# Performance work log

Measured on AMD Instinct MI355X. Metric: run time of the kernel, lower is better.

The kernel has to match this reference:

```python
import jax, jax.numpy as jnp
import numpy as np

B, N, D, H, C = 32, 512, 256, 256, 2
EPS_NEIGH = 0.3
VSN = 1e-12
SMOOTH_R, DEGREE_R, SPARSITY_R = 0.2, 0.0, 0.1


def setup_inputs() -> dict:
    key = jax.random.key(0)
    ks = jax.random.split(key, 12)
    s = 0.02
    return {
        "context": jax.random.normal(ks[0], (B, N, D), jnp.float32),
        "attention_mask": jnp.ones((B, N, 1), jnp.int32),
        "W_gcn": jax.random.normal(ks[1], (D, H), jnp.float32) * s,
        "b_gcn": jnp.zeros((H,), jnp.float32),
        "W_att1": jax.random.normal(ks[2], (H, H), jnp.float32) * s,
        "b_att1": jnp.zeros((H,), jnp.float32),
        "ln_g": jnp.ones((H,), jnp.float32),
        "ln_b": jnp.zeros((H,), jnp.float32),
        "W_att2": jax.random.normal(ks[3], (H, 1), jnp.float32) * s,
        "b_att2": jnp.zeros((1,), jnp.float32),
        "W_out": jax.random.normal(ks[4], (H, C), jnp.float32) * s,
        "b_out": jnp.zeros((C,), jnp.float32),
    }


def reference(context, attention_mask, W_gcn, b_gcn, W_att1, b_att1,
              ln_g, ln_b, W_att2, b_att2, W_out, b_out):
    # --- GraphLearner (cosine metric + epsilon neighbourhood) ---
    cn = context / jnp.maximum(
        jnp.linalg.norm(context, axis=-1, keepdims=True), VSN)
    att = jnp.einsum('bnd,bmd->bnm', cn, cn)              # [B,N,N]
    mask = jax.lax.stop_gradient((att > EPS_NEIGH).astype(att.dtype))
    adj = att * mask                                      # markoff_value = 0

    # --- GCN diffusion (row-normalized adjacency) ---
    row = adj.sum(-1, keepdims=True)                      # [B,N,1]
    adj_norm = adj / (row + VSN)
    h = jax.nn.relu(
        jnp.einsum('bnm,bmd->bnd', adj_norm, context) @ W_gcn + b_gcn)

    # --- AttentionNetPooling: Linear -> LayerNorm -> GELU -> Linear(1) ---
    a = h @ W_att1 + b_att1
    mu = a.mean(-1, keepdims=True)
    var = a.var(-1, keepdims=True)
    a = (a - mu) / jnp.sqrt(var + 1e-5) * ln_g + ln_b
    w = jax.nn.gelu(a, approximate=False) @ W_att2 + b_att2   # [B,N,1]
    w = jnp.where(attention_mask == 0, -jnp.inf, w)
    w = jax.nn.softmax(w, axis=1)
    pooled = jnp.sum(w * h, axis=1)                       # [B,H]
    logits = pooled @ W_out + b_out                       # [B,C]

    # --- add_batch_graph_loss (L = diag(rowsum) - adj, topk = N) ---
    Lx = row * context - jnp.einsum('bnm,bmd->bnd', adj, context)
    smooth = SMOOTH_R * jnp.mean(
        jnp.sum(context * Lx, axis=(-1, -2)) / (N * N))
    deg = -DEGREE_R * jnp.mean(
        jnp.sum(jnp.log(row[..., 0] + VSN), axis=-1) / N)
    sparsity = SPARSITY_R * jnp.sum(adj ** 2) / (N * N) / B
    graph_loss = smooth + deg + sparsity
    return logits, graph_loss
```

## Files before the change

### kernel.cpp

```cpp
#include <hip/hip_runtime.h>
#include <math.h>

#define NS 512
#define ND 256
#define LIST_CAP 32768u

typedef short short8 __attribute__((ext_vector_type(8)));
typedef float f32x16 __attribute__((ext_vector_type(16)));

__device__ __forceinline__ unsigned short bf16_rne(float x) {
  unsigned u = __float_as_uint(x);
  unsigned r = u + 0x7fffu + ((u >> 16) & 1u);
  return (unsigned short)(r >> 16);
}
__device__ __forceinline__ float bf16_tof(unsigned short h) {
  return __uint_as_float(((unsigned)h) << 16);
}
__device__ __forceinline__ void bsplit(float x, unsigned short& h, unsigned short& l) {
  h = bf16_rne(x);
  l = bf16_rne(x - bf16_tof(h));
}
__device__ __forceinline__ float wave_sum(float v) {
  v += __shfl_xor(v, 1);  v += __shfl_xor(v, 2);  v += __shfl_xor(v, 4);
  v += __shfl_xor(v, 8);  v += __shfl_xor(v, 16); v += __shfl_xor(v, 32);
  return v;
}

__device__ __forceinline__ void gload_lds16(const void* g, void* l) {
  __builtin_amdgcn_global_load_lds(
      (const __attribute__((address_space(1))) unsigned int*)g,
      (__attribute__((address_space(3))) unsigned int*)l, 16, 0, 0);
}

__device__ __forceinline__ void stage4(const unsigned short* __restrict__ hiA,
                                       const unsigned short* __restrict__ loA, int grA,
                                       const unsigned short* __restrict__ hiB,
                                       const unsigned short* __restrict__ loB, int grB,
                                       int k0, char* lds, int wid, int lane)
{
  #pragma unroll
  for (int q = 0; q < 2; ++q) {
    const int c = (q * 4 + wid) * 64 + lane;
    const int row = c >> 3;
    const int soff = ((c & 7) * 16) ^ ((row & 7) << 4);
    const int dest = (q * 4 + wid) * 1024;
    const size_t ga = (size_t)(grA + row) * ND + k0 + (soff >> 1);
    const size_t gb = (size_t)(grB + row) * ND + k0 + (soff >> 1);
    gload_lds16(hiA + ga, lds + dest);
    gload_lds16(loA + ga, lds + 8192 + dest);
    gload_lds16(hiB + gb, lds + 16384 + dest);
    gload_lds16(loB + gb, lds + 24576 + dest);
  }
}

#define SWZB(row, off) (((row) << 7) + (((off) ^ (((row) & 7) << 4))))

#define STEP_MFMA(lds, arow, brow) do { \
  _Pragma("unroll") \
  for (int ks = 0; ks < 4; ++ks) { \
    const int off = ks * 32 + hl * 16; \
    short8 ah = *(const short8*)((lds) + SWZB((arow), off)); \
    short8 al = *(const short8*)((lds) + 8192 + SWZB((arow), off)); \
    short8 bh = *(const short8*)((lds) + 16384 + SWZB((brow), off)); \
    short8 bl = *(const short8*)((lds) + 24576 + SWZB((brow), off)); \
    acc = __builtin_amdgcn_mfma_f32_32x32x16_bf16(ah, bh, acc, 0, 0, 0); \
    acc = __builtin_amdgcn_mfma_f32_32x32x16_bf16(ah, bl, acc, 0, 0, 0); \
    acc = __builtin_amdgcn_mfma_f32_32x32x16_bf16(al, bh, acc, 0, 0, 0); \
  } \
} while (0)

__device__ __forceinline__ float pdot_raw(const float* __restrict__ ctx,
                                          const float* __restrict__ Wg,
                                          int row, int t) {
  const float* cr = ctx + (size_t)row * ND;
  float a = 0.f;
  #pragma unroll 16
  for (int k = 0; k < ND; ++k) a = fmaf(cr[k], Wg[(size_t)k * ND + t], a);
  return a;
}

__global__ __launch_bounds__(256)
void k_prep(const float* __restrict__ ctx, const float* __restrict__ Wg,
            const float* __restrict__ Wa,
            float* __restrict__ nrm, float* __restrict__ nsq,
            unsigned short* __restrict__ cnhi, unsigned short* __restrict__ cnlo,
            unsigned short* __restrict__ wgthi, unsigned short* __restrict__ wgtlo,
            unsigned short* __restrict__ wathi, unsigned short* __restrict__ watlo,
            unsigned* __restrict__ cnt)
{
  if (blockIdx.x >= 4096) {
    int wb = blockIdx.x - 4096;
    int j = wb & 255, selA = wb >> 8;
    int k = threadIdx.x;
    if (wb == 0 && k == 0) *cnt = 0u;
    const float* W = selA ? Wa : Wg;
    unsigned short h, l;
    bsplit(W[k * ND + j], h, l);
    if (selA) { wathi[j * ND + k] = h; watlo[j * ND + k] = l; }
    else      { wgthi[j * ND + k] = h; wgtlo[j * ND + k] = l; }
    return;
  }
  int w = threadIdx.x >> 6, lane = threadIdx.x & 63;
  int g = blockIdx.x * 4 + w;
  float4 v = ((const float4*)ctx)[(size_t)g * 64 + lane];
  float ss = v.x*v.x + v.y*v.y + v.z*v.z + v.w*v.w;
  ss = wave_sum(ss);
  float n = sqrtf(ss);
  float rn = 1.f / fmaxf(n, 1e-12f);
  if (lane == 0) { nrm[g] = n; nsq[g] = ss; }
  ushort4 hi, lo;
  bsplit(v.x * rn, hi.x, lo.x);
  bsplit(v.y * rn, hi.y, lo.y);
  bsplit(v.z * rn, hi.z, lo.z);
  bsplit(v.w * rn, hi.w, lo.w);
  ((ushort4*)cnhi)[(size_t)g * 64 + lane] = hi;
  ((ushort4*)cnlo)[(size_t)g * 64 + lane] = lo;
}

__global__ __launch_bounds__(256, 4)
void k_gram2(const unsigned short* __restrict__ cnhi, const unsigned short* __restrict__ cnlo,
             const float* __restrict__ nrm,
             float* __restrict__ rowp, float* __restrict__ diag,
             float* __restrict__ pA2, float* __restrict__ pA3,
             unsigned* __restrict__ cnt, unsigned* __restrict__ keys,
             float* __restrict__ vals)
{
  __shared__ __align__(16) char lds[32768];
  __shared__ float s_row[2][64];
  __shared__ float s_col[2][64];
  __shared__ float sred[8];
  const int bx0 = blockIdx.x;
  const int bx = (bx0 & 7) * 144 + (bx0 >> 3);
  const int b = bx / 36;
  int rem = bx % 36, ti = 0;
  #pragma unroll
  for (int q = 0; q < 7; ++q) { if (rem >= 8 - ti) { rem -= 8 - ti; ++ti; } }
  const int tj = ti + rem;
  const bool diagT = (ti == tj);
  const int i0 = ti * 64, j0 = tj * 64;
  const int bB = b * NS;
  const int rbA = bB + i0, rbB = bB + j0;

  const int tid = threadIdx.x;
  const int lane = tid & 63, wid = tid >> 6;
  const int l31 = lane & 31, hl = lane >> 5;
  const int wr = wid >> 1, wc = wid & 1;
  const int arow = wr * 32 + l31;
  const int brow = wc * 32 + l31;

  f32x16 acc = {};
  #pragma unroll
  for (int t = 0; t < 4; ++t) {
    stage4(cnhi, cnlo, rbA, cnhi, cnlo, rbB, t * 64, lds, wid, lane);
    __syncthreads();
    STEP_MFMA(lds, arow, brow);
    __syncthreads();
  }

  const float nc = nrm[rbB + wc * 32 + l31];
  const int gcol = wc * 32 + l31;
  float a2 = 0.f, a3 = 0.f, colsum = 0.f;

  #pragma unroll
  for (int r = 0; r < 16; ++r) {
    const int rofs = (r & 3) + 8 * (r >> 2) + 4 * hl;
    const int grow = wr * 32 + rofs;
    const float nr = nrm[rbA + grow];
    float v = acc[r];
    float adj = (v > 0.3f) ? v : 0.f;
    float q2 = adj * adj;
    a3 += q2;
    a2 += q2 * nr * nc;
    colsum += adj;
    if (diagT) {
      if (grow == gcol) {
        diag[bB + i0 + grow] = adj;
      } else if (adj > 0.f) {
        unsigned idx = atomicAdd(cnt, 1u);
        if (idx < LIST_CAP) {
          keys[idx] = (unsigned)((bB + i0 + grow) * NS + (j0 + gcol));
          vals[idx] = adj;
        }
      }
    } else if (adj > 0.f) {
      unsigned idx = atomicAdd(cnt, 2u);
      if (idx < LIST_CAP) {
        keys[idx] = (unsigned)((bB + i0 + grow) * NS + (j0 + gcol));
        vals[idx] = adj;
      }
      if (idx + 1u < LIST_CAP) {
        keys[idx + 1u] = (unsigned)((bB + j0 + gcol) * NS + (i0 + grow));
        vals[idx + 1u] = adj;
      }
    }
    float rs = adj;
    rs += __shfl_xor(rs, 1); rs += __shfl_xor(rs, 2); rs += __shfl_xor(rs, 4);
    rs += __shfl_xor(rs, 8); rs += __shfl_xor(rs, 16);
    if (l31 == 0) s_row[wc][grow] = rs;
  }
  colsum += __shfl_xor(colsum, 32);
  if (!diagT && hl == 0) s_col[wr][gcol] = colsum;
  a2 = wave_sum(a2);
  a3 = wave_sum(a3);
  if (lane == 0) { sred[wid] = a2; sred[4 + wid] = a3; }
  __syncthreads();
  if (tid < 64) {
    rowp[tj * 16384 + rbA + tid] = s_row[0][tid] + s_row[1][tid];
    if (!diagT)
      rowp[ti * 16384 + rbB + tid] = s_col[0][tid] + s_col[1][tid];
  }
  if (tid == 0) {
    float f = diagT ? 1.f : 2.f;
    pA2[bx] = f * (sred[0] + sred[1] + sred[2] + sred[3]);
    pA3[bx] = f * (sred[4] + sred[5] + sred[6] + sred[7]);
  }
}

__global__ __launch_bounds__(256, 4)
void k_pgemm(const unsigned short* __restrict__ cnhi, const unsigned short* __restrict__ cnlo,
             const unsigned short* __restrict__ wgthi, const unsigned short* __restrict__ wgtlo,
             const float* __restrict__ rowp, const float* __restrict__ nrm,
             const float* __restrict__ nsq, const float* __restrict__ diag,
             const float* __restrict__ b_gcn,
             unsigned short* __restrict__ Hhi, unsigned short* __restrict__ Hlo,
             float* __restrict__ pA1)
{
  __shared__ __align__(16) char lds[32768];
  __shared__ float lss[64];
  const int i0 = blockIdx.x * 64;
  const int c0 = blockIdx.y * 64;
  const int tid = threadIdx.x;
  const int lane = tid & 63, wid = tid >> 6;
  const int l31 = lane & 31, hl = lane >> 5;
  const int wr = wid >> 1, wc = wid & 1;
  const int arow = wr * 32 + l31;
  const int brow = wc * 32 + l31;

  if (tid < 64) {
    int g = i0 + tid;
    float r = 0.f;
    #pragma unroll
    for (int s2 = 0; s2 < 8; ++s2) r += rowp[s2 * 16384 + g];
    float rr = 1.f / (r + 1e-12f);
    lss[tid] = nrm[g] * diag[g] * rr;
    float v = r * nsq[g];
    v = wave_sum(v);
    if (tid == 0 && blockIdx.y == 0) pA1[blockIdx.x] = v;
  }

  f32x16 acc = {};
  #pragma unroll
  for (int t = 0; t < 4; ++t) {
    stage4(cnhi, cnlo, i0, wgthi, wgtlo, c0, t * 64, lds, wid, lane);
    __syncthreads();
    STEP_MFMA(lds, arow, brow);
    __syncthreads();
  }

  const int gcol = c0 + wc * 32 + l31;
  const float bv = b_gcn[gcol];
  #pragma unroll
  for (int r = 0; r < 16; ++r) {
    const int rofs = (r & 3) + 8 * (r >> 2) + 4 * hl;
    const int lrow = wr * 32 + rofs;
    const size_t grow = (size_t)(i0 + lrow);
    float v = fmaxf(lss[lrow] * acc[r] + bv, 0.f);
    unsigned short h, l;
    bsplit(v, h, l);
    Hhi[grow * ND + gcol] = h;
    Hlo[grow * ND + gcol] = l;
  }
}

__global__ __launch_bounds__(256)
void k_fix(const float* __restrict__ ctx, const float* __restrict__ Wg,
           const float* __restrict__ rowp, const float* __restrict__ diag,
           const float* __restrict__ b_gcn,
           const unsigned* __restrict__ cnt, const unsigned* __restrict__ keys,
           const float* __restrict__ vals,
           unsigned short* __restrict__ Hhi, unsigned short* __restrict__ Hlo)
{
  unsigned c = *cnt; if (c > LIST_CAP) c = LIST_CAP;
  unsigned e = blockIdx.x;
  if (e >= c) return;
  int bn = (int)(keys[e] >> 9);
  for (unsigned e2 = 0; e2 < e; ++e2)
    if ((int)(keys[e2] >> 9) == bn) return;
  int t = threadIdx.x;
  float r = 0.f;
  #pragma unroll
  for (int s2 = 0; s2 < 8; ++s2) r += rowp[s2 * 16384 + bn];
  float rr = 1.f / (r + 1e-12f);
  float pre = diag[bn] * rr * pdot_raw(ctx, Wg, bn, t) + b_gcn[t];
  for (unsigned e2 = e; e2 < c; ++e2) {
    unsigned k2 = keys[e2];
    if ((int)(k2 >> 9) != bn) continue;
    int bm = (bn & ~511) | (int)(k2 & 511u);
    pre += vals[e2] * rr * pdot_raw(ctx, Wg, bm, t);
  }
  float hv = fmaxf(pre, 0.f);
  unsigned short hh, ll;
  bsplit(hv, hh, ll);
  Hhi[(size_t)bn * ND + t] = hh;
  Hlo[(size_t)bn * ND + t] = ll;
}

__global__ __launch_bounds__(256, 4)
void k_mm1(const unsigned short* __restrict__ Ahi, const unsigned short* __restrict__ Alo,
           const unsigned short* __restrict__ Bthi, const unsigned short* __restrict__ Btlo,
           const float* __restrict__ bias, float* __restrict__ outf)
{
  __shared__ __align__(16) char lds[32768];
  const int i0 = blockIdx.x * 64;
  const int c0 = blockIdx.y * 64;
  const int tid = threadIdx.x;
  const int lane = tid & 63, wid = tid >> 6;
  const int l31 = lane & 31, hl = lane >> 5;
  const int wr = wid >> 1, wc = wid & 1;
  const int arow = wr * 32 + l31;
  const int brow = wc * 32 + l31;

  f32x16 acc = {};
  #pragma unroll
  for (int t = 0; t < 4; ++t) {
    stage4(Ahi, Alo, i0, Bthi, Btlo, c0, t * 64, lds, wid, lane);
    __syncthreads();
    STEP_MFMA(lds, arow, brow);
    __syncthreads();
  }

  const int gcol = c0 + wc * 32 + l31;
  const float bv = bias[gcol];
  #pragma unroll
  for (int r = 0; r < 16; ++r) {
    const int rofs = (r & 3) + 8 * (r >> 2) + 4 * hl;
    const size_t grow = (size_t)(i0 + wr * 32 + rofs);
    outf[grow * ND + gcol] = acc[r] + bv;
  }
}

__global__ __launch_bounds__(256)
void k_ln(const float* __restrict__ a, const float* __restrict__ g,
          const float* __restrict__ bt, const float* __restrict__ W2,
          const float* __restrict__ b2, float* __restrict__ wl)
{
  int w = threadIdx.x >> 6, lane = threadIdx.x & 63;
  int row = blockIdx.x * 4 + w;
  float4 x = ((const float4*)a)[(size_t)row * 64 + lane];
  float s = x.x + x.y + x.z + x.w;
  float ss = fmaf(x.x, x.x, fmaf(x.y, x.y, fmaf(x.z, x.z, x.w * x.w)));
  s = wave_sum(s); ss = wave_sum(ss);
  float mu = s * (1.f / 256.f);
  float var = ss * (1.f / 256.f) - mu * mu;
  float rstd = rsqrtf(fmaxf(var, 0.f) + 1e-5f);
  float4 gg = ((const float4*)g)[lane];
  float4 bb = ((const float4*)bt)[lane];
  float4 wv = ((const float4*)W2)[lane];
  const float inv_sqrt2 = 0.70710678118654752f;
  float d = 0.f;
  float y = (x.x - mu) * rstd * gg.x + bb.x;
  d = fmaf(0.5f * y * (1.f + erff(y * inv_sqrt2)), wv.x, d);
  y = (x.y - mu) * rstd * gg.y + bb.y;
  d = fmaf(0.5f * y * (1.f + erff(y * inv_sqrt2)), wv.y, d);
  y = (x.z - mu) * rstd * gg.z + bb.z;
  d = fmaf(0.5f * y * (1.f + erff(y * inv_sqrt2)), wv.z, d);
  y = (x.w - mu) * rstd * gg.w + bb.w;
  d = fmaf(0.5f * y * (1.f + erff(y * inv_sqrt2)), wv.w, d);
  d = wave_sum(d);
  if (lane == 0) wl[row] = d + b2[0];
}

__global__ __launch_bounds__(256)
void k_pool2(const float* __restrict__ wl, const int* __restrict__ amask,
             const unsigned short* __restrict__ hhi, const unsigned short* __restrict__ hlo,
             float* __restrict__ part)
{
  __shared__ float sw[512];
  __shared__ float red[256];
  int b = blockIdx.x >> 4, p = blockIdx.x & 15, t = threadIdx.x;
  float l0 = (amask[b * NS + t]       == 0) ? -INFINITY : wl[b * NS + t];
  float l1 = (amask[b * NS + 256 + t] == 0) ? -INFINITY : wl[b * NS + 256 + t];
  red[t] = fmaxf(l0, l1);
  __syncthreads();
  for (int s = 128; s; s >>= 1) { if (t < s) red[t] = fmaxf(red[t], red[t + s]); __syncthreads(); }
  float mx = red[0];
  __syncthreads();
  float e0 = expf(l0 - mx), e1 = expf(l1 - mx);
  red[t] = e0 + e1;
  __syncthreads();
  for (int s = 128; s; s >>= 1) { if (t < s) red[t] += red[t + s]; __syncthreads(); }
  float inv = 1.f / red[0];
  sw[t] = e0 * inv; sw[256 + t] = e1 * inv;
  __syncthreads();
  const size_t base = (size_t)b * NS * ND + (size_t)p * 32 * ND + t;
  float acc = 0.f;
  #pragma unroll 8
  for (int n = 0; n < 32; ++n) {
    float hv = bf16_tof(hhi[base + (size_t)n * ND]) + bf16_tof(hlo[base + (size_t)n * ND]);
    acc = fmaf(sw[p * 32 + n], hv, acc);
  }
  part[(size_t)blockIdx.x * ND + t] = acc;
}

__global__ __launch_bounds__(256)
void k_final(const float* __restrict__ part, const float* __restrict__ W_out,
             const float* __restrict__ b_out, const float* __restrict__ pA1,
             const float* __restrict__ pA2, const float* __restrict__ pA3,
             float* __restrict__ out)
{
  __shared__ float red[512];
  int t = threadIdx.x;
  if (blockIdx.x < 32) {
    int b = blockIdx.x;
    float pl = 0.f;
    #pragma unroll
    for (int p = 0; p < 16; ++p) pl += part[(size_t)(b * 16 + p) * ND + t];
    red[t]       = pl * W_out[t * 2 + 0];
    red[256 + t] = pl * W_out[t * 2 + 1];
    __syncthreads();
    for (int s = 128; s; s >>= 1) {
      if (t < s) { red[t] += red[t + s]; red[256 + t] += red[256 + t + s]; }
      __syncthreads();
    }
    if (t == 0) {
      out[b * 2 + 0] = red[0]   + b_out[0];
      out[b * 2 + 1] = red[256] + b_out[1];
    }
  } else {
    float r1 = pA1[t];
    float r2 = 0.f, r3 = 0.f;
    #pragma unroll
    for (int i = 0; i < 5; ++i) {
      int idx = i * 256 + t;
      if (idx < 1152) { r2 += pA2[idx]; r3 += pA3[idx]; }
    }
    red[t] = r1; red[256 + t] = r2;
    __syncthreads();
    for (int s = 128; s; s >>= 1) {
      if (t < s) { red[t] += red[t + s]; red[256 + t] += red[256 + t + s]; }
      __syncthreads();
    }
    r1 = red[0]; r2 = red[256];
    __syncthreads();
    red[t] = r3;
    __syncthreads();
    for (int s = 128; s; s >>= 1) { if (t < s) red[t] += red[t + s]; __syncthreads(); }
    if (t == 0) {
      float smooth = 0.2f * (r1 - r2) * (1.f / (32.f * 512.f * 512.f));
      float spars  = 0.1f * red[0] * (1.f / (512.f * 512.f)) * (1.f / 32.f);
      out[64] = smooth + spars;
    }
  }
}

extern "C" void kernel_launch(void* const* d_in, const int* in_sizes, int n_in,
                              void* d_out, int out_size, void* d_ws, size_t ws_size,
                              hipStream_t stream)
{
  (void)in_sizes; (void)n_in; (void)out_size; (void)ws_size;
  const float* ctx    = (const float*)d_in[0];
  const int*   amask  = (const int*)d_in[1];
  const float* W_gcn  = (const float*)d_in[2];
  const float* b_gcn  = (const float*)d_in[3];
  const float* W_att1 = (const float*)d_in[4];
  const float* b_att1 = (const float*)d_in[5];
  const float* ln_g   = (const float*)d_in[6];
  const float* ln_b   = (const float*)d_in[7];
  const float* W_att2 = (const float*)d_in[8];
  const float* b_att2 = (const float*)d_in[9];
  const float* W_out  = (const float*)d_in[10];
  const float* b_out  = (const float*)d_in[11];
  float* out = (float*)d_out;

  float* ws = (float*)d_ws;
  unsigned short* cnhi = (unsigned short*)ws;
  unsigned short* cnlo = (unsigned short*)(ws + 2097152);
  float* part = ws;
  unsigned short* Hhi  = (unsigned short*)(ws + 4194304);
  unsigned short* Hlo  = (unsigned short*)(ws + 4194304 + 2097152);
  float* abuf = ws + 8388608;
  float* sp   = ws + 12582912;
  float* nrm  = sp;            sp += 16384;
  float* nsq  = sp;            sp += 16384;
  float* rowp = sp;            sp += 131072;
  float* diag = sp;            sp += 16384;
  float* wl   = sp;            sp += 16384;
  float* pA1  = sp;            sp += 4096;
  float* pA2  = sp;            sp += 1280;
  float* pA3  = sp;            sp += 1280;
  unsigned* cnt  = (unsigned*)sp;  sp += 64;
  unsigned* keys = (unsigned*)sp;  sp += 32768;
  float* vals = sp;            sp += 32768;
  unsigned short* wgthi = (unsigned short*)sp; sp += 32768;
  unsigned short* wgtlo = (unsigned short*)sp; sp += 32768;
  unsigned short* wathi = (unsigned short*)sp; sp += 32768;
  unsigned short* watlo = (unsigned short*)sp; sp += 32768;

  k_prep<<<4608, 256, 0, stream>>>(ctx, W_gcn, W_att1, nrm, nsq, cnhi, cnlo,
                                   wgthi, wgtlo, wathi, watlo, cnt);
  k_gram2<<<1152, 256, 0, stream>>>(cnhi, cnlo, nrm, rowp, diag, pA2, pA3,
                                    cnt, keys, vals);
  k_pgemm<<<dim3(256, 4), 256, 0, stream>>>(cnhi, cnlo, wgthi, wgtlo, rowp,
                                            nrm, nsq, diag, b_gcn, Hhi, Hlo, pA1);
  k_fix<<<256, 256, 0, stream>>>(ctx, W_gcn, rowp, diag, b_gcn,
                                 cnt, keys, vals, Hhi, Hlo);
  k_mm1<<<dim3(256, 4), 256, 0, stream>>>(Hhi, Hlo, wathi, watlo, b_att1, abuf);
  k_ln<<<4096, 256, 0, stream>>>(abuf, ln_g, ln_b, W_att2, b_att2, wl);
  k_pool2<<<512, 256, 0, stream>>>(wl, amask, Hhi, Hlo, part);
  k_final<<<33, 256, 0, stream>>>(part, W_out, b_out, pA1, pA2, pA3, out);
}
```

Before: 89.96 us.

## Double-buffer LDS staging in split-bf16 MFMA GEMM kernels

The three MFMA GEMM kernels now use a 64KB LDS ping-pong buffer, staging the next K-slice while the current one feeds the MFMAs. This halves the number of barriers and overlaps global loads with matrix math. The price is double the LDS per block, so the occupancy hint drops from 4 to 2 blocks per CU. The weight-transpose prep also swaps its thread and block index roles so that reads from W become coalesced while the transposed writes become strided.

```diff
diff --git a/kernel.cpp b/kernel.cpp
--- a/kernel.cpp
+++ b/kernel.cpp
@@ -69,6 +69,21 @@
   } \
 } while (0)
 
+#define KLOOP_2PH(hiA, loA, grA, hiB, loB, grB) do { \
+  stage4(hiA, loA, grA, hiB, loB, grB, 0, lds, wid, lane); \
+  __syncthreads(); \
+  stage4(hiA, loA, grA, hiB, loB, grB, 64, lds + 32768, wid, lane); \
+  STEP_MFMA(lds, arow, brow); \
+  __syncthreads(); \
+  stage4(hiA, loA, grA, hiB, loB, grB, 128, lds, wid, lane); \
+  STEP_MFMA(lds + 32768, arow, brow); \
+  __syncthreads(); \
+  stage4(hiA, loA, grA, hiB, loB, grB, 192, lds + 32768, wid, lane); \
+  STEP_MFMA(lds, arow, brow); \
+  __syncthreads(); \
+  STEP_MFMA(lds + 32768, arow, brow); \
+} while (0)
+
 __device__ __forceinline__ float pdot_raw(const float* __restrict__ ctx,
                                           const float* __restrict__ Wg,
                                           int row, int t) {
@@ -90,9 +105,9 @@
 {
   if (blockIdx.x >= 4096) {
     int wb = blockIdx.x - 4096;
-    int j = wb & 255, selA = wb >> 8;
-    int k = threadIdx.x;
-    if (wb == 0 && k == 0) *cnt = 0u;
+    int k = wb & 255, selA = wb >> 8;
+    int j = threadIdx.x;
+    if (wb == 0 && j == 0) *cnt = 0u;
     const float* W = selA ? Wa : Wg;
     unsigned short h, l;
     bsplit(W[k * ND + j], h, l);
@@ -117,7 +132,7 @@
   ((ushort4*)cnlo)[(size_t)g * 64 + lane] = lo;
 }
 
-__global__ __launch_bounds__(256, 4)
+__global__ __launch_bounds__(256, 2)
 void k_gram2(const unsigned short* __restrict__ cnhi, const unsigned short* __restrict__ cnlo,
              const float* __restrict__ nrm,
              float* __restrict__ rowp, float* __restrict__ diag,
@@ -125,7 +140,7 @@
              unsigned* __restrict__ cnt, unsigned* __restrict__ keys,
              float* __restrict__ vals)
 {
-  __shared__ __align__(16) char lds[32768];
+  __shared__ __align__(16) char lds[65536];
   __shared__ float s_row[2][64];
   __shared__ float s_col[2][64];
   __shared__ float sred[8];
@@ -149,13 +164,7 @@
   const int brow = wc * 32 + l31;
 
   f32x16 acc = {};
-  #pragma unroll
-  for (int t = 0; t < 4; ++t) {
-    stage4(cnhi, cnlo, rbA, cnhi, cnlo, rbB, t * 64, lds, wid, lane);
-    __syncthreads();
-    STEP_MFMA(lds, arow, brow);
-    __syncthreads();
-  }
+  KLOOP_2PH(cnhi, cnlo, rbA, cnhi, cnlo, rbB);
 
   const float nc = nrm[rbB + wc * 32 + l31];
   const int gcol = wc * 32 + l31;
@@ -216,7 +225,7 @@
   }
 }
 
-__global__ __launch_bounds__(256, 4)
+__global__ __launch_bounds__(256, 2)
 void k_pgemm(const unsigned short* __restrict__ cnhi, const unsigned short* __restrict__ cnlo,
              const unsigned short* __restrict__ wgthi, const unsigned short* __restrict__ wgtlo,
              const float* __restrict__ rowp, const float* __restrict__ nrm,
@@ -225,7 +234,7 @@
              unsigned short* __restrict__ Hhi, unsigned short* __restrict__ Hlo,
              float* __restrict__ pA1)
 {
-  __shared__ __align__(16) char lds[32768];
+  __shared__ __align__(16) char lds[65536];
   __shared__ float lss[64];
   const int i0 = blockIdx.x * 64;
   const int c0 = blockIdx.y * 64;
@@ -249,13 +258,7 @@
   }
 
   f32x16 acc = {};
-  #pragma unroll
-  for (int t = 0; t < 4; ++t) {
-    stage4(cnhi, cnlo, i0, wgthi, wgtlo, c0, t * 64, lds, wid, lane);
-    __syncthreads();
-    STEP_MFMA(lds, arow, brow);
-    __syncthreads();
-  }
+  KLOOP_2PH(cnhi, cnlo, i0, wgthi, wgtlo, c0);
 
   const int gcol = c0 + wc * 32 + l31;
   const float bv = b_gcn[gcol];
@@ -305,12 +308,12 @@
   Hlo[(size_t)bn * ND + t] = ll;
 }
 
-__global__ __launch_bounds__(256, 4)
+__global__ __launch_bounds__(256, 2)
 void k_mm1(const unsigned short* __restrict__ Ahi, const unsigned short* __restrict__ Alo,
            const unsigned short* __restrict__ Bthi, const unsigned short* __restrict__ Btlo,
            const float* __restrict__ bias, float* __restrict__ outf)
 {
-  __shared__ __align__(16) char lds[32768];
+  __shared__ __align__(16) char lds[65536];
   const int i0 = blockIdx.x * 64;
   const int c0 = blockIdx.y * 64;
   const int tid = threadIdx.x;
@@ -321,13 +324,7 @@
   const int brow = wc * 32 + l31;
 
   f32x16 acc = {};
-  #pragma unroll
-  for (int t = 0; t < 4; ++t) {
-    stage4(Ahi, Alo, i0, Bthi, Btlo, c0, t * 64, lds, wid, lane);
-    __syncthreads();
-    STEP_MFMA(lds, arow, brow);
-    __syncthreads();
-  }
+  KLOOP_2PH(Ahi, Alo, i0, Bthi, Btlo, c0);
 
   const int gcol = c0 + wc * 32 + l31;
   const float bv = bias[gcol];
```

Result: slower. 97.56 us (+8.4%).
